# Performance work log

Hardware: AMD Instinct MI355X
Metric: run time of the kernel (lower is better)

## Reference

```python
import jax, jax.numpy as jnp
import numpy as np

WIN = (8, 8)
NUM_HEADS = 8
DIM = 256


def _relative_position_index(wh, ww):
    ch = np.arange(wh)
    cw = np.arange(ww)
    coords = np.stack(np.meshgrid(ch, cw, indexing='ij'))  # [2, wh, ww]
    cf = coords.reshape(2, -1)                              # [2, N]
    rel = cf[:, :, None] - cf[:, None, :]                   # [2, N, N]
    rel = rel.transpose(1, 2, 0).copy()
    rel[:, :, 0] += wh - 1
    rel[:, :, 1] += ww - 1
    rel[:, :, 0] *= 2 * ww - 1
    return rel.sum(-1).astype(np.int32)                     # [N, N]


def setup_inputs() -> dict:
    key = jax.random.key(0)
    ks = jax.random.split(key, 7)
    N = WIN[0] * WIN[1]
    BW = 4096  # num_windows * batch
    x = jax.random.normal(ks[0], (BW, N, DIM), dtype=jnp.float32)
    # 0 / -inf style shift mask; random 0 or -100 per entry for generality
    mask = jnp.where(jax.random.uniform(ks[1], (BW, N, N)) < 0.2, -100.0, 0.0).astype(jnp.float32)
    rpb_table = jax.random.normal(ks[2], ((2 * WIN[0] - 1) * (2 * WIN[1] - 1), NUM_HEADS), dtype=jnp.float32) * 0.02
    qkv_w = jax.random.normal(ks[3], (3 * DIM, DIM), dtype=jnp.float32) * (DIM ** -0.5)
    qkv_b = jax.random.normal(ks[4], (3 * DIM,), dtype=jnp.float32) * 0.01
    proj_w = jax.random.normal(ks[5], (DIM, DIM), dtype=jnp.float32) * (DIM ** -0.5)
    proj_b = jax.random.normal(ks[6], (DIM,), dtype=jnp.float32) * 0.01
    rel_idx = jnp.asarray(_relative_position_index(*WIN))
    return {"x": x, "mask": mask, "rpb_table": rpb_table, "qkv_w": qkv_w,
            "qkv_b": qkv_b, "proj_w": proj_w, "proj_b": proj_b, "rel_idx": rel_idx}


def reference(x, mask, rpb_table, qkv_w, qkv_b, proj_w, proj_b, rel_idx):
    B_, N, C = x.shape
    H = NUM_HEADS
    hd = C // H
    scale = hd ** -0.5
    qkv = x @ qkv_w.T + qkv_b                               # [B_, N, 3C]
    qkv = qkv.reshape(B_, N, 3, H, hd).transpose(2, 0, 3, 1, 4)  # [3, B_, H, N, hd]
    q, k, v = qkv[0], qkv[1], qkv[2]
    attn = jnp.einsum('bhnd,bhmd->bhnm', q * scale, k)      # [B_, H, N, N]
    bias = rpb_table[rel_idx.reshape(-1)].reshape(N, N, H).transpose(2, 0, 1)  # [H, N, N]
    attn = attn + bias[None]
    nW = mask.shape[0]
    attn = attn.reshape(B_ // nW, nW, H, N, N) + mask[None, :, None]
    attn = attn.reshape(B_, H, N, N)
    attn = jax.nn.softmax(attn, axis=-1)
    out = jnp.einsum('bhnm,bhmd->bhnd', attn, v)            # [B_, H, N, hd]
    out = out.transpose(0, 2, 1, 3).reshape(B_, N, C)
    return out @ proj_w.T + proj_b
```

## Files before the change

kernel.cpp:

```cpp
#include <hip/hip_runtime.h>

typedef _Float16 half_t;
typedef __attribute__((ext_vector_type(4))) _Float16 half4;
typedef __attribute__((ext_vector_type(8))) _Float16 half8;
typedef __attribute__((ext_vector_type(4))) float f32x4;

#define WS_W1   0
#define WS_W2   (768*256*2)
#define WS_BIAS (WS_W2 + 256*256*2)
#define QK_SCALE 0.17677669529663687f

__global__ __launch_bounds__(256) void prep_kernel(
    const float* __restrict__ qkv_w, const float* __restrict__ proj_w,
    const float* __restrict__ rpb, const int* __restrict__ rel_idx,
    char* __restrict__ ws) {
  int tid = blockIdx.x * 256 + threadIdx.x;
  half_t* W1 = (half_t*)(ws + WS_W1);
  half_t* W2 = (half_t*)(ws + WS_W2);
  float* BIASP = (float*)(ws + WS_BIAS);
  if (tid < 768 * 256) {
    int n = tid >> 8;
    float v = qkv_w[tid];
    if (n < 256) v *= QK_SCALE;
    W1[tid] = (half_t)v;
  }
  if (tid < 256 * 256) W2[tid] = (half_t)proj_w[tid];
  if (tid < 8 * 4096) {
    int r   = tid & 3;
    int l16 = (tid >> 2) & 15;
    int q   = (tid >> 6) & 3;
    int nt  = (tid >> 8) & 3;
    int mt  = (tid >> 10) & 3;
    int h   = (tid >> 12) & 7;
    int i = 16 * mt + 4 * q + r;
    int j = 16 * nt + l16;
    BIASP[tid] = rpb[rel_idx[i * 64 + j] * 8 + h];
  }
}

__device__ __forceinline__ void qkv_gemm(const half_t* Xs, const half_t* W1,
                                         int n0, int l16, int quad,
                                         f32x4 acc[2][4]) {
#pragma unroll
  for (int ks = 0; ks < 8; ++ks) {
    half8 af[4];
#pragma unroll
    for (int mt = 0; mt < 4; ++mt)
      af[mt] = *(const half8*)(&Xs[(16 * mt + l16) * 264 + 32 * ks + quad * 8]);
#pragma unroll
    for (int nt = 0; nt < 2; ++nt) {
      half8 bf = *(const half8*)(&W1[(size_t)(n0 + 16 * nt + l16) * 256 + 32 * ks + quad * 8]);
#pragma unroll
      for (int mt = 0; mt < 4; ++mt)
        acc[nt][mt] = __builtin_amdgcn_mfma_f32_16x16x32_f16(af[mt], bf, acc[nt][mt], 0, 0, 0);
    }
  }
}

__global__ __attribute__((amdgpu_flat_work_group_size(512, 512),
                          amdgpu_waves_per_eu(4, 4))) void fused_kernel(
    const float* __restrict__ x, const float* __restrict__ mask,
    const float* __restrict__ qkv_b, const float* __restrict__ proj_b,
    const char* __restrict__ ws, float* __restrict__ out, int nW) {
  __shared__ __align__(16) half_t Xs[64 * 264];
  __shared__ __align__(16) half_t Ms[64 * 68];
  __shared__ __align__(16) half_t Scr[8][2304];

  const int b = blockIdx.x;
  const int tid = threadIdx.x;
  const int wave = tid >> 6, lane = tid & 63;
  const int l16 = lane & 15, quad = lane >> 4;
  const f32x4 z4 = {0.f, 0.f, 0.f, 0.f};
  const half_t* W1 = (const half_t*)(ws + WS_W1);
  half_t* Sw = &Scr[wave][0];

  {
    const float4* xw = (const float4*)(x + (size_t)b * 16384);
#pragma unroll
    for (int i = 0; i < 8; ++i) {
      int idx4 = tid + i * 512;
      float4 v = xw[idx4];
      int e = idx4 << 2;
      int row = e >> 8, col = e & 255;
      half4 pk;
      pk[0] = (half_t)v.x; pk[1] = (half_t)v.y; pk[2] = (half_t)v.z; pk[3] = (half_t)v.w;
      *(half4*)(&Xs[row * 264 + col]) = pk;
    }
    const float4* mw = (const float4*)(mask + (size_t)(b % nW) * 4096);
#pragma unroll
    for (int i = 0; i < 2; ++i) {
      int idx4 = tid + i * 512;
      float4 v = mw[idx4];
      int e = idx4 << 2;
      int mi = e >> 6, mj = e & 63;
      half4 pk;
      pk[0] = (half_t)v.x; pk[1] = (half_t)v.y; pk[2] = (half_t)v.z; pk[3] = (half_t)v.w;
      *(half4*)(&Ms[mi * 68 + mj]) = pk;
    }
  }
  __syncthreads();

  const int h = wave;
  half8 vf[2][2];
  half8 qf[4];
  half8 kf[4];
  half4 oh[4][2];

  {
    f32x4 acc[2][4];
#pragma unroll
    for (int nt = 0; nt < 2; ++nt)
#pragma unroll
      for (int mt = 0; mt < 4; ++mt) acc[nt][mt] = z4;
    const int n0 = 512 + 32 * h;
    qkv_gemm(Xs, W1, n0, l16, quad, acc);
#pragma unroll
    for (int nt = 0; nt < 2; ++nt) {
      float vb = qkv_b[n0 + 16 * nt + l16];
#pragma unroll
      for (int mt = 0; mt < 4; ++mt) {
        half4 pk;
#pragma unroll
        for (int r = 0; r < 4; ++r) pk[r] = (half_t)(acc[nt][mt][r] + vb);
        *(half4*)(&Sw[(16 * nt + l16) * 72 + 16 * mt + 4 * quad]) = pk;
      }
    }
#pragma unroll
    for (int nt = 0; nt < 2; ++nt)
#pragma unroll
      for (int ks = 0; ks < 2; ++ks)
        vf[nt][ks] = *(const half8*)(&Sw[(16 * nt + l16) * 72 + 32 * ks + quad * 8]);
    asm volatile("s_waitcnt lgkmcnt(0)" ::: "memory");
  }

  {
    f32x4 acc[2][4];
#pragma unroll
    for (int nt = 0; nt < 2; ++nt)
#pragma unroll
      for (int mt = 0; mt < 4; ++mt) acc[nt][mt] = z4;
    const int n0 = 32 * h;
    qkv_gemm(Xs, W1, n0, l16, quad, acc);
#pragma unroll
    for (int nt = 0; nt < 2; ++nt) {
      float qb = qkv_b[n0 + 16 * nt + l16] * QK_SCALE;
#pragma unroll
      for (int mt = 0; mt < 4; ++mt)
#pragma unroll
        for (int r = 0; r < 4; ++r)
          Sw[(16 * mt + 4 * quad + r) * 36 + 16 * nt + l16] = (half_t)(acc[nt][mt][r] + qb);
    }
#pragma unroll
    for (int mt = 0; mt < 4; ++mt) {
      union { half8 v; half4 hh[2]; } u;
      u.hh[0] = *(const half4*)(&Sw[(16 * mt + l16) * 36 + quad * 8]);
      u.hh[1] = *(const half4*)(&Sw[(16 * mt + l16) * 36 + quad * 8 + 4]);
      qf[mt] = u.v;
    }
    asm volatile("s_waitcnt lgkmcnt(0)" ::: "memory");
  }

  {
    f32x4 acc[2][4];
#pragma unroll
    for (int nt = 0; nt < 2; ++nt)
#pragma unroll
      for (int mt = 0; mt < 4; ++mt) acc[nt][mt] = z4;
    const int n0 = 256 + 32 * h;
    qkv_gemm(Xs, W1, n0, l16, quad, acc);
#pragma unroll
    for (int nt = 0; nt < 2; ++nt) {
      float kb = qkv_b[n0 + 16 * nt + l16];
#pragma unroll
      for (int mt = 0; mt < 4; ++mt)
#pragma unroll
        for (int r = 0; r < 4; ++r)
          Sw[(16 * mt + 4 * quad + r) * 36 + 16 * nt + l16] = (half_t)(acc[nt][mt][r] + kb);
    }
#pragma unroll
    for (int jt = 0; jt < 4; ++jt) {
      union { half8 v; half4 hh[2]; } u;
      u.hh[0] = *(const half4*)(&Sw[(16 * jt + l16) * 36 + quad * 8]);
      u.hh[1] = *(const half4*)(&Sw[(16 * jt + l16) * 36 + quad * 8 + 4]);
      kf[jt] = u.v;
    }
    asm volatile("s_waitcnt lgkmcnt(0)" ::: "memory");
  }

  {
    const float4* BP4 = (const float4*)(ws + WS_BIAS);
#pragma unroll
    for (int mt = 0; mt < 4; ++mt) {
      f32x4 St[4];
#pragma unroll
      for (int nt = 0; nt < 4; ++nt)
        St[nt] = __builtin_amdgcn_mfma_f32_16x16x32_f16(qf[mt], kf[nt], z4, 0, 0, 0);
#pragma unroll
      for (int nt = 0; nt < 4; ++nt) {
        float4 bv = BP4[(size_t)(((h * 4 + mt) * 4 + nt) * 64) + quad * 16 + l16];
#pragma unroll
        for (int r = 0; r < 4; ++r)
          St[nt][r] += ((const float*)&bv)[r] +
                       (float)Ms[(16 * mt + 4 * quad + r) * 68 + 16 * nt + l16];
      }
      float linv[4];
#pragma unroll
      for (int r = 0; r < 4; ++r) {
        float mx = fmaxf(fmaxf(St[0][r], St[1][r]), fmaxf(St[2][r], St[3][r]));
#pragma unroll
        for (int o = 1; o < 16; o <<= 1) mx = fmaxf(mx, __shfl_xor(mx, o, 64));
        float s = 0.f;
#pragma unroll
        for (int nt = 0; nt < 4; ++nt) {
          float e = exp2f((St[nt][r] - mx) * 1.44269504f);
          St[nt][r] = e;
          s += e;
        }
#pragma unroll
        for (int o = 1; o < 16; o <<= 1) s += __shfl_xor(s, o, 64);
        linv[r] = __builtin_amdgcn_rcpf(s);
      }
#pragma unroll
      for (int nt = 0; nt < 4; ++nt)
#pragma unroll
        for (int r = 0; r < 4; ++r)
          Sw[(4 * quad + r) * 72 + 16 * nt + l16] = (half_t)St[nt][r];
      f32x4 o0 = z4, o1 = z4;
#pragma unroll
      for (int ks = 0; ks < 2; ++ks) {
        half8 pf = *(const half8*)(&Sw[l16 * 72 + 32 * ks + quad * 8]);
        o0 = __builtin_amdgcn_mfma_f32_16x16x32_f16(pf, vf[0][ks], o0, 0, 0, 0);
        o1 = __builtin_amdgcn_mfma_f32_16x16x32_f16(pf, vf[1][ks], o1, 0, 0, 0);
      }
#pragma unroll
      for (int r = 0; r < 4; ++r) {
        oh[mt][0][r] = (half_t)(o0[r] * linv[r]);
        oh[mt][1][r] = (half_t)(o1[r] * linv[r]);
      }
      asm volatile("s_waitcnt lgkmcnt(0)" ::: "memory");
    }
  }
  __syncthreads();

#pragma unroll
  for (int mt = 0; mt < 4; ++mt)
#pragma unroll
    for (int nt = 0; nt < 2; ++nt)
#pragma unroll
      for (int r = 0; r < 4; ++r)
        Xs[(16 * mt + 4 * quad + r) * 264 + 32 * h + 16 * nt + l16] = oh[mt][nt][r];
  __syncthreads();

  {
    const half_t* W2 = (const half_t*)(ws + WS_W2);
    const int nb = wave * 32;
    f32x4 C[2][4];
#pragma unroll
    for (int nt = 0; nt < 2; ++nt)
#pragma unroll
      for (int mt = 0; mt < 4; ++mt) C[nt][mt] = z4;
#pragma unroll
    for (int ks = 0; ks < 8; ++ks) {
      half8 af[4];
#pragma unroll
      for (int mt = 0; mt < 4; ++mt)
        af[mt] = *(const half8*)(&Xs[(16 * mt + l16) * 264 + 32 * ks + quad * 8]);
#pragma unroll
      for (int nt = 0; nt < 2; ++nt) {
        half8 bf = *(const half8*)(&W2[(size_t)(nb + 16 * nt + l16) * 256 + 32 * ks + quad * 8]);
#pragma unroll
        for (int mt = 0; mt < 4; ++mt)
          C[nt][mt] = __builtin_amdgcn_mfma_f32_16x16x32_f16(af[mt], bf, C[nt][mt], 0, 0, 0);
      }
    }
#pragma unroll
    for (int nt = 0; nt < 2; ++nt) {
      int c = nb + 16 * nt + l16;
      float pb = proj_b[c];
#pragma unroll
      for (int mt = 0; mt < 4; ++mt)
#pragma unroll
        for (int r = 0; r < 4; ++r) {
          int t = 16 * mt + 4 * quad + r;
          out[(size_t)b * 16384 + t * 256 + c] = C[nt][mt][r] + pb;
        }
    }
  }
}

extern "C" void kernel_launch(void* const* d_in, const int* in_sizes, int n_in,
                              void* d_out, int out_size, void* d_ws, size_t ws_size,
                              hipStream_t stream) {
  const float* x      = (const float*)d_in[0];
  const float* mask   = (const float*)d_in[1];
  const float* rpb    = (const float*)d_in[2];
  const float* qkv_w  = (const float*)d_in[3];
  const float* qkv_b  = (const float*)d_in[4];
  const float* proj_w = (const float*)d_in[5];
  const float* proj_b = (const float*)d_in[6];
  const int*   rel    = (const int*)d_in[7];
  float* out = (float*)d_out;
  char* ws = (char*)d_ws;
  int B_ = in_sizes[0] / 16384;
  int nW = in_sizes[1] / 4096;
  hipLaunchKernelGGL(prep_kernel, dim3(768), dim3(256), 0, stream,
                     qkv_w, proj_w, rpb, rel, ws);
  hipLaunchKernelGGL(fused_kernel, dim3(B_), dim3(512), 0, stream,
                     x, mask, qkv_b, proj_b, (const char*)ws, out, nW);
}
```

Before: 820.8 us.

## Compute transposed attention scores so softmax probabilities feed PV MFMA from registers

Swaps the MFMA operand order for QK^T so each lane holds a column of scores for one query row. The softmax max and sum then need only two cross-lane shuffles instead of four per row. The exponentiated probabilities and the V projection output are kept in registers as 16x16x16 MFMA operands, which removes the LDS round-trips for P and V. The bias table is re-permuted in prep to match, and output stores become vectorized half4 writes. In exchange it uses twice as many, smaller 16x16x16 MFMAs for PV and adds some register pressure.

```diff
diff --git a/kernel.cpp b/kernel.cpp
--- a/kernel.cpp
+++ b/kernel.cpp
@@ -32,8 +32,8 @@
     int nt  = (tid >> 8) & 3;
     int mt  = (tid >> 10) & 3;
     int h   = (tid >> 12) & 7;
-    int i = 16 * mt + 4 * q + r;
-    int j = 16 * nt + l16;
+    int i = 16 * mt + l16;
+    int j = 16 * nt + 4 * q + r;
     BIASP[tid] = rpb[rel_idx[i * 64 + j] * 8 + h];
   }
 }
@@ -101,10 +101,9 @@
   __syncthreads();
 
   const int h = wave;
-  half8 vf[2][2];
+  half4 vh[2][4];
   half8 qf[4];
   half8 kf[4];
-  half4 oh[4][2];
 
   {
     f32x4 acc[2][4];
@@ -118,19 +117,11 @@
     for (int nt = 0; nt < 2; ++nt) {
       float vb = qkv_b[n0 + 16 * nt + l16];
 #pragma unroll
-      for (int mt = 0; mt < 4; ++mt) {
-        half4 pk;
-#pragma unroll
-        for (int r = 0; r < 4; ++r) pk[r] = (half_t)(acc[nt][mt][r] + vb);
-        *(half4*)(&Sw[(16 * nt + l16) * 72 + 16 * mt + 4 * quad]) = pk;
-      }
-    }
-#pragma unroll
-    for (int nt = 0; nt < 2; ++nt)
-#pragma unroll
-      for (int ks = 0; ks < 2; ++ks)
-        vf[nt][ks] = *(const half8*)(&Sw[(16 * nt + l16) * 72 + 32 * ks + quad * 8]);
-    asm volatile("s_waitcnt lgkmcnt(0)" ::: "memory");
+      for (int mt = 0; mt < 4; ++mt)
+#pragma unroll
+        for (int r = 0; r < 4; ++r)
+          vh[nt][mt][r] = (half_t)(acc[nt][mt][r] + vb);
+    }
   }
 
   {
@@ -184,71 +175,65 @@
       u.hh[1] = *(const half4*)(&Sw[(16 * jt + l16) * 36 + quad * 8 + 4]);
       kf[jt] = u.v;
     }
-    asm volatile("s_waitcnt lgkmcnt(0)" ::: "memory");
-  }
-
+  }
+
+  half4 oh[4][2];
   {
     const float4* BP4 = (const float4*)(ws + WS_BIAS);
 #pragma unroll
-    for (int mt = 0; mt < 4; ++mt) {
-      f32x4 St[4];
-#pragma unroll
-      for (int nt = 0; nt < 4; ++nt)
-        St[nt] = __builtin_amdgcn_mfma_f32_16x16x32_f16(qf[mt], kf[nt], z4, 0, 0, 0);
-#pragma unroll
-      for (int nt = 0; nt < 4; ++nt) {
-        float4 bv = BP4[(size_t)(((h * 4 + mt) * 4 + nt) * 64) + quad * 16 + l16];
-#pragma unroll
-        for (int r = 0; r < 4; ++r)
-          St[nt][r] += ((const float*)&bv)[r] +
-                       (float)Ms[(16 * mt + 4 * quad + r) * 68 + 16 * nt + l16];
-      }
-      float linv[4];
+    for (int it = 0; it < 4; ++it) {
+      f32x4 Sj[4];
+#pragma unroll
+      for (int jt = 0; jt < 4; ++jt)
+        Sj[jt] = __builtin_amdgcn_mfma_f32_16x16x32_f16(kf[jt], qf[it], z4, 0, 0, 0);
+#pragma unroll
+      for (int jt = 0; jt < 4; ++jt) {
+        float4 bv = BP4[(size_t)(((h * 4 + it) * 4 + jt) * 64) + quad * 16 + l16];
+        half4 mk = *(const half4*)(&Ms[(16 * it + l16) * 68 + 16 * jt + 4 * quad]);
+#pragma unroll
+        for (int r = 0; r < 4; ++r)
+          Sj[jt][r] += ((const float*)&bv)[r] + (float)mk[r];
+      }
+      float mx = Sj[0][0];
+#pragma unroll
+      for (int jt = 0; jt < 4; ++jt)
+#pragma unroll
+        for (int r = 0; r < 4; ++r) mx = fmaxf(mx, Sj[jt][r]);
+      mx = fmaxf(mx, __shfl_xor(mx, 16, 64));
+      mx = fmaxf(mx, __shfl_xor(mx, 32, 64));
+      float s = 0.f;
+      half4 ph[4];
+#pragma unroll
+      for (int jt = 0; jt < 4; ++jt)
+#pragma unroll
+        for (int r = 0; r < 4; ++r) {
+          float e = exp2f((Sj[jt][r] - mx) * 1.44269504f);
+          s += e;
+          ph[jt][r] = (half_t)e;
+        }
+      s += __shfl_xor(s, 16, 64);
+      s += __shfl_xor(s, 32, 64);
+      float linv = __builtin_amdgcn_rcpf(s);
+      f32x4 o0 = z4, o1 = z4;
+#pragma unroll
+      for (int jt = 0; jt < 4; ++jt) {
+        o0 = __builtin_amdgcn_mfma_f32_16x16x16f16(vh[0][jt], ph[jt], o0, 0, 0, 0);
+        o1 = __builtin_amdgcn_mfma_f32_16x16x16f16(vh[1][jt], ph[jt], o1, 0, 0, 0);
+      }
 #pragma unroll
       for (int r = 0; r < 4; ++r) {
-        float mx = fmaxf(fmaxf(St[0][r], St[1][r]), fmaxf(St[2][r], St[3][r]));
-#pragma unroll
-        for (int o = 1; o < 16; o <<= 1) mx = fmaxf(mx, __shfl_xor(mx, o, 64));
-        float s = 0.f;
-#pragma unroll
-        for (int nt = 0; nt < 4; ++nt) {
-          float e = exp2f((St[nt][r] - mx) * 1.44269504f);
-          St[nt][r] = e;
-          s += e;
-        }
-#pragma unroll
-        for (int o = 1; o < 16; o <<= 1) s += __shfl_xor(s, o, 64);
-        linv[r] = __builtin_amdgcn_rcpf(s);
-      }
-#pragma unroll
-      for (int nt = 0; nt < 4; ++nt)
-#pragma unroll
-        for (int r = 0; r < 4; ++r)
-          Sw[(4 * quad + r) * 72 + 16 * nt + l16] = (half_t)St[nt][r];
-      f32x4 o0 = z4, o1 = z4;
-#pragma unroll
-      for (int ks = 0; ks < 2; ++ks) {
-        half8 pf = *(const half8*)(&Sw[l16 * 72 + 32 * ks + quad * 8]);
-        o0 = __builtin_amdgcn_mfma_f32_16x16x32_f16(pf, vf[0][ks], o0, 0, 0, 0);
-        o1 = __builtin_amdgcn_mfma_f32_16x16x32_f16(pf, vf[1][ks], o1, 0, 0, 0);
-      }
-#pragma unroll
-      for (int r = 0; r < 4; ++r) {
-        oh[mt][0][r] = (half_t)(o0[r] * linv[r]);
-        oh[mt][1][r] = (half_t)(o1[r] * linv[r]);
-      }
-      asm volatile("s_waitcnt lgkmcnt(0)" ::: "memory");
+        oh[it][0][r] = (half_t)(o0[r] * linv);
+        oh[it][1][r] = (half_t)(o1[r] * linv);
+      }
     }
   }
   __syncthreads();
 
 #pragma unroll
-  for (int mt = 0; mt < 4; ++mt)
-#pragma unroll
-    for (int nt = 0; nt < 2; ++nt)
-#pragma unroll
-      for (int r = 0; r < 4; ++r)
-        Xs[(16 * mt + 4 * quad + r) * 264 + 32 * h + 16 * nt + l16] = oh[mt][nt][r];
+  for (int it = 0; it < 4; ++it)
+#pragma unroll
+    for (int dt = 0; dt < 2; ++dt)
+      *(half4*)(&Xs[(16 * it + l16) * 264 + 32 * h + 16 * dt + 4 * quad]) = oh[it][dt];
   __syncthreads();
 
   {
```

Measured after the change: 829.2 us. About the same (+1.0%).
